# Optimization experiments

Measured on AMD Instinct MI355X. Metric: run time of the kernel, lower is better.

## Reference

```python
import jax, jax.numpy as jnp
import numpy as np
import math

NUM_HEADS = 8

def _ln(x, g, b, eps=1e-5):
    mu = x.mean(-1, keepdims=True)
    var = ((x - mu) ** 2).mean(-1, keepdims=True)
    return (x - mu) / jnp.sqrt(var + eps) * g + b

def setup_inputs() -> dict:
    key = jax.random.key(0)
    ks = jax.random.split(key, 10)
    B, Nq, Nk, dQ, dK, dV = 16, 1024, 1024, 512, 512, 512
    s = 0.05  # small init so the double-exp in masked_softmax stays finite
    Q = jax.random.normal(ks[0], (B, Nq, dQ), jnp.float32)
    K = jax.random.normal(ks[1], (B, Nk, dK), jnp.float32)
    Qm = (jax.random.uniform(ks[2], (B, Nq, 1)) < 0.9).astype(jnp.float32)
    Km = (jax.random.uniform(ks[3], (B, Nk, 1)) < 0.9).astype(jnp.float32)
    Wq = jax.random.normal(ks[4], (dQ, dV), jnp.float32) * s
    Wk = jax.random.normal(ks[5], (dK, dV), jnp.float32) * s
    Wv = jax.random.normal(ks[6], (dK, dV), jnp.float32) * s
    Wo = jax.random.normal(ks[7], (dV, dV), jnp.float32) * s
    bq = jnp.zeros((dV,), jnp.float32); bk = jnp.zeros((dV,), jnp.float32)
    bv = jnp.zeros((dV,), jnp.float32); bo = jnp.zeros((dV,), jnp.float32)
    g0 = jnp.ones((dV,), jnp.float32); b0 = jnp.zeros((dV,), jnp.float32)
    g1 = jnp.ones((dV,), jnp.float32); b1 = jnp.zeros((dV,), jnp.float32)
    return {"Q": Q, "K": K, "Qm": Qm, "Km": Km,
            "Wq": Wq, "bq": bq, "Wk": Wk, "bk": bk, "Wv": Wv, "bv": bv,
            "Wo": Wo, "bo": bo, "g0": g0, "b0": b0, "g1": g1, "b1": b1}

def reference(Q, K, Qm, Km, Wq, bq, Wk, bk, Wv, bv, Wo, bo, g0, b0, g1, b1):
    B, Nq, _ = Q.shape
    Nk = K.shape[1]
    dV = Wq.shape[1]
    h = NUM_HEADS
    dh = dV // h
    # projections + feature masking (Qm/Km broadcast over feature dim)
    Qp = (Q @ Wq + bq) * Qm          # [B,Nq,dV]
    Kp = (K @ Wk + bk) * Km          # [B,Nk,dV]
    V  = K @ Wv + bv                 # [B,Nk,dV]
    # head split: torch.cat(split(dh,2),0) == head-major [h,B,N,dh]
    Qh = Qp.reshape(B, Nq, h, dh).transpose(2, 0, 1, 3)
    Kh = Kp.reshape(B, Nk, h, dh).transpose(2, 0, 1, 3)
    Vh = V.reshape(B, Nk, h, dh).transpose(2, 0, 1, 3)
    S = jnp.einsum('hbqd,hbkd->hbqk', Qh, Kh) / math.sqrt(dV)
    # faithful masked_softmax: exp applied twice (Km branch then Qm branch)
    X = jnp.exp(S) * Km[:, :, 0][None, :, None, :]   # [h,B,Nq,Nk]
    X = jnp.exp(X) * Qm[:, :, 0][None, :, :, None]
    A = X / (X.sum(-1, keepdims=True) + 1e-8)
    O = Qh + jnp.einsum('hbqk,hbkd->hbqd', A, Vh)    # residual in head space
    O = O.transpose(1, 2, 0, 3).reshape(B, Nq, dV)   # merge heads back
    O = _ln(O, g0, b0)
    O = O + jax.nn.relu(O @ Wo + bo)
    return _ln(O, g1, b1)
```

## Files before the change

kernel.cpp:

```cpp
#include <hip/hip_runtime.h>
#include <hip/hip_bf16.h>
#include <cstdint>


typedef __bf16 bf16;
typedef __bf16 bf16x4 __attribute__((ext_vector_type(4)));
typedef __bf16 bf16x8 __attribute__((ext_vector_type(8)));
typedef float f32x4 __attribute__((ext_vector_type(4)));

#define MFMA16(a, b, c) __builtin_amdgcn_mfma_f32_16x16x32_bf16((a), (b), (c), 0, 0, 0)

#if __has_builtin(__builtin_amdgcn_exp2f)
#define EXP2F(x) __builtin_amdgcn_exp2f(x)
#else
#define EXP2F(x) exp2f(x)
#endif

static __device__ __forceinline__ void async_lds16(const bf16* g, bf16* l) {
  __builtin_amdgcn_global_load_lds(
      (__attribute__((address_space(1))) void*)(void*)g,
      (__attribute__((address_space(3))) void*)l,
      16, 0, 0);
}

__global__ __launch_bounds__(256) void transposeW(
    const float* __restrict__ Wq, const float* __restrict__ Wk,
    const float* __restrict__ Wv, const float* __restrict__ Wo,
    bf16* __restrict__ Tq, bf16* __restrict__ Tk,
    bf16* __restrict__ Tv, bf16* __restrict__ To) {
  const float* src;
  bf16* dst;
  switch (blockIdx.z) {
    case 0: src = Wq; dst = Tq; break;
    case 1: src = Wk; dst = Tk; break;
    case 2: src = Wv; dst = Tv; break;
    default: src = Wo; dst = To; break;
  }
  __shared__ bf16 t[64][72];
  const int tid = threadIdx.x;
  const int n0 = blockIdx.x * 64;
  const int k0 = blockIdx.y * 64;
  for (int c = tid; c < 512; c += 256) {
    const int row = c >> 3, col = (c & 7) * 8;
    const float* sp = src + (size_t)(k0 + row) * 512 + n0 + col;
    const f32x4 a = *(const f32x4*)sp;
    const f32x4 b = *(const f32x4*)(sp + 4);
    bf16x8 v;
#pragma unroll
    for (int j = 0; j < 4; ++j) { v[j] = (bf16)a[j]; v[j + 4] = (bf16)b[j]; }
    *(bf16x8*)(&t[row][col]) = v;
  }
  __syncthreads();
  for (int c = tid; c < 512; c += 256) {
    const int row = c >> 3, col8 = (c & 7) * 8;
    bf16x8 v;
#pragma unroll
    for (int j = 0; j < 8; ++j) v[j] = t[col8 + j][row];
    *(bf16x8*)(dst + (size_t)(n0 + row) * 512 + k0 + col8) = v;
  }
}

struct ConvArgs {
  const float* src[10];
  bf16* dst[10];
  int n[10];
};

__global__ __launch_bounds__(256) void convert_all(ConvArgs a) {
  const int seg = blockIdx.z;
  const int n = a.n[seg];
  const long i = ((long)blockIdx.x * 256 + threadIdx.x) * 8;
  if (i >= n) return;
  const float* s = a.src[seg];
  const f32x4 x0 = *(const f32x4*)(s + i);
  const f32x4 x1 = *(const f32x4*)(s + i + 4);
  bf16x8 o;
#pragma unroll
  for (int j = 0; j < 4; ++j) { o[j] = (bf16)x0[j]; o[j + 4] = (bf16)x1[j]; }
  *(bf16x8*)(a.dst[seg] + i) = o;
}

template <bool AF32>
__global__ __launch_bounds__(256, 2) void gemm512(
    const void* __restrict__ A, const bf16* __restrict__ Bt,
    const bf16* __restrict__ bias, const bf16* __restrict__ mask,
    const bf16* __restrict__ resid, bf16* __restrict__ out) {
  __shared__ bf16 sA[128 * 32];
  __shared__ bf16 sB[128 * 32];
  const int tid = threadIdx.x;
  const int lane = tid & 63;
  const int w = tid >> 6;
  const int fm = lane & 15;
  const int fq = lane >> 4;
  const long rowBase = (long)blockIdx.y * 128;
  const int colBase = blockIdx.x * 128;

  f32x4 acc[4][4] = {};

  const int c0 = tid, c1 = tid + 256;
  const int r0 = c0 >> 2, o0 = (c0 & 3) * 8;
  const int r1 = c1 >> 2, o1 = (c1 & 3) * 8;
  const bf16* A0 = (const bf16*)A + (rowBase + r0) * 512 + o0;
  const bf16* A1 = (const bf16*)A + (rowBase + r1) * 512 + o1;
  const float* F0 = (const float*)A + (rowBase + r0) * 512 + o0;
  const float* F1 = (const float*)A + (rowBase + r1) * 512 + o1;
  const bf16* B0 = Bt + (size_t)(colBase + r0) * 512 + o0;
  const bf16* B1 = Bt + (size_t)(colBase + r1) * 512 + o1;

  const int wr = (w & 1) * 64;
  const int wc = (w >> 1) * 64;

  f32x4 nx0, nx1, ny0, ny1;
  if (AF32) {
    nx0 = *(const f32x4*)(F0);
    nx1 = *(const f32x4*)(F0 + 4);
    ny0 = *(const f32x4*)(F1);
    ny1 = *(const f32x4*)(F1 + 4);
  }

  for (int kt = 0; kt < 16; ++kt) {
    const int k0 = kt * 32;
    __syncthreads();
    if (AF32) {
      bf16x8 p, q;
#pragma unroll
      for (int j = 0; j < 4; ++j) {
        p[j] = (bf16)nx0[j]; p[j + 4] = (bf16)nx1[j];
        q[j] = (bf16)ny0[j]; q[j + 4] = (bf16)ny1[j];
      }
      *(bf16x8*)(sA + c0 * 8) = p;
      *(bf16x8*)(sA + c1 * 8) = q;
      if (kt < 15) {
        nx0 = *(const f32x4*)(F0 + k0 + 32);
        nx1 = *(const f32x4*)(F0 + k0 + 36);
        ny0 = *(const f32x4*)(F1 + k0 + 32);
        ny1 = *(const f32x4*)(F1 + k0 + 36);
      }
    } else {
      async_lds16(A0 + k0, sA + c0 * 8);
      async_lds16(A1 + k0, sA + c1 * 8);
    }
    async_lds16(B0 + k0, sB + c0 * 8);
    async_lds16(B1 + k0, sB + c1 * 8);
    __syncthreads();
    bf16x8 a[4], b[4];
#pragma unroll
    for (int i = 0; i < 4; ++i)
      a[i] = *(const bf16x8*)(sA + (wr + i * 16 + fm) * 32 + fq * 8);
#pragma unroll
    for (int j = 0; j < 4; ++j)
      b[j] = *(const bf16x8*)(sB + (wc + j * 16 + fm) * 32 + fq * 8);
#pragma unroll
    for (int i = 0; i < 4; ++i)
#pragma unroll
      for (int j = 0; j < 4; ++j)
        acc[i][j] = MFMA16(a[i], b[j], acc[i][j]);
  }

#pragma unroll
  for (int i = 0; i < 4; ++i) {
#pragma unroll
    for (int r = 0; r < 4; ++r) {
      const long R = rowBase + wr + i * 16 + fq * 4 + r;
      const float mk = mask ? (float)mask[R] : 1.0f;
      const bf16* resrow = resid ? resid + R * 512 : nullptr;
      bf16* outrow = out + R * 512;
#pragma unroll
      for (int j = 0; j < 4; ++j) {
        const int C = colBase + wc + j * 16 + fm;
        float v = acc[i][j][r] + (float)bias[C];
        if (mask) v *= mk;
        if (resid) v = (float)resrow[C] + fmaxf(v, 0.0f);
        outrow[C] = (bf16)v;
      }
    }
  }
}

__global__ __launch_bounds__(256, 2) void gemmKV(
    const float* __restrict__ A, const bf16* __restrict__ Btk,
    const bf16* __restrict__ Btv, const bf16* __restrict__ bk,
    const bf16* __restrict__ bv, const bf16* __restrict__ Km,
    bf16* __restrict__ Kp, bf16* __restrict__ Vt) {
  __shared__ bf16 sA[128 * 32];
  __shared__ bf16 sBk[128 * 32];
  __shared__ bf16 sBv[128 * 32];
  const int tid = threadIdx.x;
  const int lane = tid & 63;
  const int w = tid >> 6;
  const int fm = lane & 15;
  const int fq = lane >> 4;
  const long rowBase = (long)blockIdx.y * 128;
  const int colBase = blockIdx.x * 128;

  f32x4 acck[4][4] = {};
  f32x4 accv[4][4] = {};

  const int c0 = tid, c1 = tid + 256;
  const int r0 = c0 >> 2, o0 = (c0 & 3) * 8;
  const int r1 = c1 >> 2, o1 = (c1 & 3) * 8;
  const float* F0 = A + (rowBase + r0) * 512 + o0;
  const float* F1 = A + (rowBase + r1) * 512 + o1;
  const bf16* Bk0 = Btk + (size_t)(colBase + r0) * 512 + o0;
  const bf16* Bk1 = Btk + (size_t)(colBase + r1) * 512 + o1;
  const bf16* Bv0 = Btv + (size_t)(colBase + r0) * 512 + o0;
  const bf16* Bv1 = Btv + (size_t)(colBase + r1) * 512 + o1;

  const int wr = (w & 1) * 64;
  const int wc = (w >> 1) * 64;

  f32x4 nx0 = *(const f32x4*)(F0);
  f32x4 nx1 = *(const f32x4*)(F0 + 4);
  f32x4 ny0 = *(const f32x4*)(F1);
  f32x4 ny1 = *(const f32x4*)(F1 + 4);

  for (int kt = 0; kt < 16; ++kt) {
    const int k0 = kt * 32;
    __syncthreads();
    {
      bf16x8 p, q;
#pragma unroll
      for (int j = 0; j < 4; ++j) {
        p[j] = (bf16)nx0[j]; p[j + 4] = (bf16)nx1[j];
        q[j] = (bf16)ny0[j]; q[j + 4] = (bf16)ny1[j];
      }
      *(bf16x8*)(sA + c0 * 8) = p;
      *(bf16x8*)(sA + c1 * 8) = q;
      if (kt < 15) {
        nx0 = *(const f32x4*)(F0 + k0 + 32);
        nx1 = *(const f32x4*)(F0 + k0 + 36);
        ny0 = *(const f32x4*)(F1 + k0 + 32);
        ny1 = *(const f32x4*)(F1 + k0 + 36);
      }
    }
    async_lds16(Bk0 + k0, sBk + c0 * 8);
    async_lds16(Bk1 + k0, sBk + c1 * 8);
    async_lds16(Bv0 + k0, sBv + c0 * 8);
    async_lds16(Bv1 + k0, sBv + c1 * 8);
    __syncthreads();
    bf16x8 a[4], b[4], bv2[4];
#pragma unroll
    for (int i = 0; i < 4; ++i)
      a[i] = *(const bf16x8*)(sA + (wr + i * 16 + fm) * 32 + fq * 8);
#pragma unroll
    for (int j = 0; j < 4; ++j) {
      b[j] = *(const bf16x8*)(sBk + (wc + j * 16 + fm) * 32 + fq * 8);
      bv2[j] = *(const bf16x8*)(sBv + (wc + j * 16 + fm) * 32 + fq * 8);
    }
#pragma unroll
    for (int i = 0; i < 4; ++i)
#pragma unroll
      for (int j = 0; j < 4; ++j) {
        acck[i][j] = MFMA16(a[i], b[j], acck[i][j]);
        accv[i][j] = MFMA16(a[i], bv2[j], accv[i][j]);
      }
  }

  const int bidx = (int)(rowBase >> 10);
#pragma unroll
  for (int i = 0; i < 4; ++i) {
#pragma unroll
    for (int r = 0; r < 4; ++r) {
      const long R = rowBase + wr + i * 16 + fq * 4 + r;
      const float mk = (float)Km[R];
      bf16* outrow = Kp + R * 512;
#pragma unroll
      for (int j = 0; j < 4; ++j) {
        const int C = colBase + wc + j * 16 + fm;
        outrow[C] = (bf16)((acck[i][j][r] + (float)bk[C]) * mk);
      }
    }
    const int kkb = (int)(rowBase & 1023) + wr + i * 16 + fq * 4;
#pragma unroll
    for (int j = 0; j < 4; ++j) {
      const int C = colBase + wc + j * 16 + fm;
      const float bvc = (float)bv[C];
      bf16x4 pv;
#pragma unroll
      for (int r = 0; r < 4; ++r) pv[r] = (bf16)(accv[i][j][r] + bvc);
      bf16* dst = Vt + ((size_t)(bidx * 8 + (C >> 6)) * 64 + (C & 63)) * 1024 + kkb;
      *(bf16x4*)((void*)dst) = pv;
    }
  }
}

__global__ __launch_bounds__(256) void attn_kernel(
    bf16* __restrict__ Qp, const bf16* __restrict__ Kp,
    const bf16* __restrict__ Vt, const bf16* __restrict__ Qm,
    const bf16* __restrict__ Km) {
  __shared__ bf16 sQ[64][72];
  __shared__ bf16 sK[64][72];
  __shared__ bf16 sVt[64][72];
  __shared__ bf16 sX[4][16][72];
  __shared__ float sKl[64];
  __shared__ float sL[4][16];

  const int tid = threadIdx.x;
  const int lane = tid & 63;
  const int w = tid >> 6;
  const int fm = lane & 15;
  const int fq = lane >> 4;
  const int id = blockIdx.x;
  const int bh = id & 127;
  const int q0 = (id >> 7) * 64;
  const int b = bh >> 3;
  const int hh = bh & 7;

  bf16* Qbase = Qp + ((long)b * 1024 + q0) * 512 + hh * 64;
  for (int c = tid; c < 512; c += 256) {
    const int row = c >> 3, col = (c & 7) * 8;
    *(bf16x8*)(&sQ[row][col]) = *(const bf16x8*)(Qbase + (long)row * 512 + col);
  }
  const float qm_lane = (float)Qm[(long)b * 1024 + q0 + w * 16 + fm];
  __syncthreads();

  bf16x8 qf[2];
  qf[0] = *(const bf16x8*)(&sQ[w * 16 + fm][fq * 8]);
  qf[1] = *(const bf16x8*)(&sQ[w * 16 + fm][32 + fq * 8]);

  f32x4 acc_o[4] = {};
  float l_lane = 0.f;
  const float c1 = 0.063758715f;
  const float LOG2E = 1.4426950408889634f;

  const bf16* Vthead = Vt + ((long)b * 8 + hh) * 64 * 1024;
  const bf16* Kbb = Kp + (long)b * 1024 * 512 + hh * 64;
  const bf16* Kmb = Km + (long)b * 1024;

  for (int kt = 0; kt < 16; ++kt) {
    const int kk0 = kt * 64;
    __syncthreads();
    const bf16* Kbase = Kbb + (long)kk0 * 512;
    for (int c = tid; c < 512; c += 256) {
      const int row = c >> 3, col = (c & 7) * 8;
      *(bf16x8*)(&sK[row][col]) = *(const bf16x8*)(Kbase + (long)row * 512 + col);
      *(bf16x8*)(&sVt[row][col]) =
          *(const bf16x8*)(Vthead + (long)row * 1024 + kk0 + col);
    }
    if (tid < 64) sKl[tid] = (float)Kmb[kk0 + tid] * LOG2E;
    __syncthreads();

    f32x4 s_acc[4] = {};
#pragma unroll
    for (int ks = 0; ks < 2; ++ks)
#pragma unroll
      for (int t = 0; t < 4; ++t) {
        const bf16x8 kf = *(const bf16x8*)(&sK[t * 16 + fm][ks * 32 + fq * 8]);
        s_acc[t] = MFMA16(kf, qf[ks], s_acc[t]);
      }
#pragma unroll
    for (int t = 0; t < 4; ++t) {
      const f32x4 kml4 = *(const f32x4*)(&sKl[t * 16 + fq * 4]);
      bf16x4 xp;
#pragma unroll
      for (int r = 0; r < 4; ++r) {
        const float e1 = EXP2F(s_acc[t][r] * c1);
        const float y = EXP2F(e1 * kml4[r]);
        l_lane += y;
        xp[r] = (bf16)y;
      }
      *(bf16x4*)((void*)&sX[w][fm][t * 16 + fq * 4]) = xp;
    }
#pragma unroll
    for (int ks = 0; ks < 2; ++ks) {
      const bf16x8 xf = *(const bf16x8*)(&sX[w][fm][ks * 32 + fq * 8]);
#pragma unroll
      for (int t = 0; t < 4; ++t) {
        const bf16x8 vf = *(const bf16x8*)(&sVt[t * 16 + fm][ks * 32 + fq * 8]);
        acc_o[t] = MFMA16(xf, vf, acc_o[t]);
      }
    }
  }

  l_lane += __shfl_xor(l_lane, 16);
  l_lane += __shfl_xor(l_lane, 32);
  if (fq == 0) sL[w][fm] = l_lane;

#pragma unroll
  for (int t = 0; t < 4; ++t) {
#pragma unroll
    for (int r = 0; r < 4; ++r) {
      const int qr = w * 16 + fq * 4 + r;
      const int dc = t * 16 + fm;
      const float qm_r = __shfl(qm_lane, fq * 4 + r, 64);
      const float li = 1.0f / (qm_r * sL[w][fq * 4 + r] + 1e-8f);
      const float val = (float)sQ[qr][dc] + qm_r * acc_o[t][r] * li;
      Qbase[(long)qr * 512 + dc] = (bf16)val;
    }
  }
}

__global__ __launch_bounds__(256) void lnorm(
    const bf16* __restrict__ X, const bf16* __restrict__ g,
    const bf16* __restrict__ bb, bf16* __restrict__ out) {
  const int row = blockIdx.x * 4 + (threadIdx.x >> 6);
  const int lane = threadIdx.x & 63;
  const bf16x8 v = *(const bf16x8*)(X + (size_t)row * 512 + lane * 8);
  float x[8], s = 0.f, ss = 0.f;
#pragma unroll
  for (int j = 0; j < 8; ++j) {
    x[j] = (float)v[j];
    s += x[j];
    ss += x[j] * x[j];
  }
#pragma unroll
  for (int m = 1; m < 64; m <<= 1) {
    s += __shfl_xor(s, m);
    ss += __shfl_xor(ss, m);
  }
  const float mean = s * (1.0f / 512.0f);
  const float var = ss * (1.0f / 512.0f) - mean * mean;
  const float rstd = 1.0f / sqrtf(var + 1e-5f);
  const bf16x8 gv = *(const bf16x8*)(g + lane * 8);
  const bf16x8 bv = *(const bf16x8*)(bb + lane * 8);
  bf16x8 o;
#pragma unroll
  for (int j = 0; j < 8; ++j)
    o[j] = (bf16)((x[j] - mean) * rstd * (float)gv[j] + (float)bv[j]);
  *(bf16x8*)(out + (size_t)row * 512 + lane * 8) = o;
}

__global__ __launch_bounds__(256) void lnorm_out(
    const bf16* __restrict__ X, const bf16* __restrict__ g,
    const bf16* __restrict__ bb, float* __restrict__ out) {
  const int row = blockIdx.x * 4 + (threadIdx.x >> 6);
  const int lane = threadIdx.x & 63;
  const bf16x8 v = *(const bf16x8*)(X + (size_t)row * 512 + lane * 8);
  float x[8], s = 0.f, ss = 0.f;
#pragma unroll
  for (int j = 0; j < 8; ++j) {
    x[j] = (float)v[j];
    s += x[j];
    ss += x[j] * x[j];
  }
#pragma unroll
  for (int m = 1; m < 64; m <<= 1) {
    s += __shfl_xor(s, m);
    ss += __shfl_xor(ss, m);
  }
  const float mean = s * (1.0f / 512.0f);
  const float var = ss * (1.0f / 512.0f) - mean * mean;
  const float rstd = 1.0f / sqrtf(var + 1e-5f);
  const bf16x8 gv = *(const bf16x8*)(g + lane * 8);
  const bf16x8 bv = *(const bf16x8*)(bb + lane * 8);
  f32x4 a, c;
#pragma unroll
  for (int j = 0; j < 4; ++j) {
    a[j] = (x[j] - mean) * rstd * (float)gv[j] + (float)bv[j];
    c[j] = (x[j + 4] - mean) * rstd * (float)gv[j + 4] + (float)bv[j + 4];
  }
  float* fo = out + (size_t)row * 512 + lane * 8;
  *(f32x4*)fo = a;
  *(f32x4*)(fo + 4) = c;
}

extern "C" void kernel_launch(void* const* d_in, const int* in_sizes, int n_in,
                              void* d_out, int out_size, void* d_ws, size_t ws_size,
                              hipStream_t stream) {
  (void)in_sizes; (void)n_in; (void)out_size; (void)ws_size;
  const float* Q = (const float*)d_in[0];
  const float* K = (const float*)d_in[1];

  bf16* ws = (bf16*)d_ws;
  const long W2 = 512L * 512;
  const long MN = 16384L * 512;
  bf16* Tq = ws;
  bf16* Tk = Tq + W2;
  bf16* Tv = Tk + W2;
  bf16* To = Tv + W2;
  bf16* sm = To + W2;
  bf16* cQm = sm + 8 * 512;
  bf16* cKm = cQm + 16384;
  bf16* Qp = cKm + 16384;
  bf16* Kp = Qp + MN;
  bf16* Vt = (bf16*)d_out;

  bf16* cbq = sm + 0 * 512;
  bf16* cbk = sm + 1 * 512;
  bf16* cbv = sm + 2 * 512;
  bf16* cbo = sm + 3 * 512;
  bf16* cg0 = sm + 4 * 512;
  bf16* cb0 = sm + 5 * 512;
  bf16* cg1 = sm + 6 * 512;
  bf16* cb1 = sm + 7 * 512;

  transposeW<<<dim3(8, 8, 4), 256, 0, stream>>>(
      (const float*)d_in[4], (const float*)d_in[6],
      (const float*)d_in[8], (const float*)d_in[10], Tq, Tk, Tv, To);

  ConvArgs ca;
  ca.src[0] = (const float*)d_in[2];  ca.dst[0] = cQm; ca.n[0] = 16384;
  ca.src[1] = (const float*)d_in[3];  ca.dst[1] = cKm; ca.n[1] = 16384;
  ca.src[2] = (const float*)d_in[5];  ca.dst[2] = cbq; ca.n[2] = 512;
  ca.src[3] = (const float*)d_in[7];  ca.dst[3] = cbk; ca.n[3] = 512;
  ca.src[4] = (const float*)d_in[9];  ca.dst[4] = cbv; ca.n[4] = 512;
  ca.src[5] = (const float*)d_in[11]; ca.dst[5] = cbo; ca.n[5] = 512;
  ca.src[6] = (const float*)d_in[12]; ca.dst[6] = cg0; ca.n[6] = 512;
  ca.src[7] = (const float*)d_in[13]; ca.dst[7] = cb0; ca.n[7] = 512;
  ca.src[8] = (const float*)d_in[14]; ca.dst[8] = cg1; ca.n[8] = 512;
  ca.src[9] = (const float*)d_in[15]; ca.dst[9] = cb1; ca.n[9] = 512;
  convert_all<<<dim3(8, 1, 10), 256, 0, stream>>>(ca);

  const dim3 gg(4, 128);
  gemm512<true><<<gg, 256, 0, stream>>>(Q, Tq, cbq, cQm, nullptr, Qp);
  gemmKV<<<gg, 256, 0, stream>>>(K, Tk, Tv, cbk, cbv, cKm, Kp, Vt);

  attn_kernel<<<2048, 256, 0, stream>>>(Qp, Kp, Vt, cQm, cKm);

  lnorm<<<4096, 256, 0, stream>>>(Qp, cg0, cb0, Qp);
  gemm512<false><<<gg, 256, 0, stream>>>(Qp, To, cbo, nullptr, Qp, Kp);
  lnorm_out<<<4096, 256, 0, stream>>>(Kp, cg1, cb1, (float*)d_out);
}
```

Before: 311.4 us.

## Pre-convert inputs to bf16, swizzle GEMM tiles, double attention query tile

A separate kernel now converts Q and K from fp32 to bf16 up front, so the projection GEMMs can load A through asynchronous global-to-LDS copies instead of converting inside the loop in registers. The GEMM blocks use a swizzled 1-D grid so that neighbouring blocks share A rows for better L2 reuse. The attention kernel processes 128 query rows per block (32 per wave) so each K/V tile loaded into LDS serves twice as many queries. The cost is an extra full read and write of Q and K in bf16, plus higher register and LDS use in the attention kernel.

```diff
diff --git a/kernel.cpp b/kernel.cpp
--- a/kernel.cpp
+++ b/kernel.cpp
@@ -21,6 +21,11 @@
       (__attribute__((address_space(1))) void*)(void*)g,
       (__attribute__((address_space(3))) void*)l,
       16, 0, 0);
+}
+
+static __device__ __forceinline__ void swz512(int id, long& rowBase, int& colBase) {
+  colBase = ((id >> 3) & 3) * 128;
+  rowBase = (long)((id & 7) + 8 * (id >> 5)) * 128;
 }
 
 __global__ __launch_bounds__(256) void transposeW(
@@ -60,6 +65,20 @@
   }
 }
 
+__global__ __launch_bounds__(256) void convertX(
+    const float* __restrict__ Q, const float* __restrict__ K,
+    bf16* __restrict__ Qb, bf16* __restrict__ Kb) {
+  const float* s = blockIdx.y ? K : Q;
+  bf16* d = blockIdx.y ? Kb : Qb;
+  const long i = ((long)blockIdx.x * 256 + threadIdx.x) * 8;
+  const f32x4 x0 = *(const f32x4*)(s + i);
+  const f32x4 x1 = *(const f32x4*)(s + i + 4);
+  bf16x8 o;
+#pragma unroll
+  for (int j = 0; j < 4; ++j) { o[j] = (bf16)x0[j]; o[j + 4] = (bf16)x1[j]; }
+  *(bf16x8*)(d + i) = o;
+}
+
 struct ConvArgs {
   const float* src[10];
   bf16* dst[10];
@@ -80,9 +99,8 @@
   *(bf16x8*)(a.dst[seg] + i) = o;
 }
 
-template <bool AF32>
 __global__ __launch_bounds__(256, 2) void gemm512(
-    const void* __restrict__ A, const bf16* __restrict__ Bt,
+    const bf16* __restrict__ A, const bf16* __restrict__ Bt,
     const bf16* __restrict__ bias, const bf16* __restrict__ mask,
     const bf16* __restrict__ resid, bf16* __restrict__ out) {
   __shared__ bf16 sA[128 * 32];
@@ -92,54 +110,27 @@
   const int w = tid >> 6;
   const int fm = lane & 15;
   const int fq = lane >> 4;
-  const long rowBase = (long)blockIdx.y * 128;
-  const int colBase = blockIdx.x * 128;
+  long rowBase; int colBase;
+  swz512(blockIdx.x, rowBase, colBase);
 
   f32x4 acc[4][4] = {};
 
   const int c0 = tid, c1 = tid + 256;
   const int r0 = c0 >> 2, o0 = (c0 & 3) * 8;
   const int r1 = c1 >> 2, o1 = (c1 & 3) * 8;
-  const bf16* A0 = (const bf16*)A + (rowBase + r0) * 512 + o0;
-  const bf16* A1 = (const bf16*)A + (rowBase + r1) * 512 + o1;
-  const float* F0 = (const float*)A + (rowBase + r0) * 512 + o0;
-  const float* F1 = (const float*)A + (rowBase + r1) * 512 + o1;
+  const bf16* A0 = A + (rowBase + r0) * 512 + o0;
+  const bf16* A1 = A + (rowBase + r1) * 512 + o1;
   const bf16* B0 = Bt + (size_t)(colBase + r0) * 512 + o0;
   const bf16* B1 = Bt + (size_t)(colBase + r1) * 512 + o1;
 
   const int wr = (w & 1) * 64;
   const int wc = (w >> 1) * 64;
-
-  f32x4 nx0, nx1, ny0, ny1;
-  if (AF32) {
-    nx0 = *(const f32x4*)(F0);
-    nx1 = *(const f32x4*)(F0 + 4);
-    ny0 = *(const f32x4*)(F1);
-    ny1 = *(const f32x4*)(F1 + 4);
-  }
 
   for (int kt = 0; kt < 16; ++kt) {
     const int k0 = kt * 32;
     __syncthreads();
-    if (AF32) {
-      bf16x8 p, q;
-#pragma unroll
-      for (int j = 0; j < 4; ++j) {
-        p[j] = (bf16)nx0[j]; p[j + 4] = (bf16)nx1[j];
-        q[j] = (bf16)ny0[j]; q[j + 4] = (bf16)ny1[j];
-      }
-      *(bf16x8*)(sA + c0 * 8) = p;
-      *(bf16x8*)(sA + c1 * 8) = q;
-      if (kt < 15) {
-        nx0 = *(const f32x4*)(F0 + k0 + 32);
-        nx1 = *(const f32x4*)(F0 + k0 + 36);
-        ny0 = *(const f32x4*)(F1 + k0 + 32);
-        ny1 = *(const f32x4*)(F1 + k0 + 36);
-      }
-    } else {
-      async_lds16(A0 + k0, sA + c0 * 8);
-      async_lds16(A1 + k0, sA + c1 * 8);
-    }
+    async_lds16(A0 + k0, sA + c0 * 8);
+    async_lds16(A1 + k0, sA + c1 * 8);
     async_lds16(B0 + k0, sB + c0 * 8);
     async_lds16(B1 + k0, sB + c1 * 8);
     __syncthreads();
@@ -178,7 +169,7 @@
 }
 
 __global__ __launch_bounds__(256, 2) void gemmKV(
-    const float* __restrict__ A, const bf16* __restrict__ Btk,
+    const bf16* __restrict__ A, const bf16* __restrict__ Btk,
     const bf16* __restrict__ Btv, const bf16* __restrict__ bk,
     const bf16* __restrict__ bv, const bf16* __restrict__ Km,
     bf16* __restrict__ Kp, bf16* __restrict__ Vt) {
@@ -190,8 +181,8 @@
   const int w = tid >> 6;
   const int fm = lane & 15;
   const int fq = lane >> 4;
-  const long rowBase = (long)blockIdx.y * 128;
-  const int colBase = blockIdx.x * 128;
+  long rowBase; int colBase;
+  swz512(blockIdx.x, rowBase, colBase);
 
   f32x4 acck[4][4] = {};
   f32x4 accv[4][4] = {};
@@ -199,8 +190,8 @@
   const int c0 = tid, c1 = tid + 256;
   const int r0 = c0 >> 2, o0 = (c0 & 3) * 8;
   const int r1 = c1 >> 2, o1 = (c1 & 3) * 8;
-  const float* F0 = A + (rowBase + r0) * 512 + o0;
-  const float* F1 = A + (rowBase + r1) * 512 + o1;
+  const bf16* A0 = A + (rowBase + r0) * 512 + o0;
+  const bf16* A1 = A + (rowBase + r1) * 512 + o1;
   const bf16* Bk0 = Btk + (size_t)(colBase + r0) * 512 + o0;
   const bf16* Bk1 = Btk + (size_t)(colBase + r1) * 512 + o1;
   const bf16* Bv0 = Btv + (size_t)(colBase + r0) * 512 + o0;
@@ -209,30 +200,11 @@
   const int wr = (w & 1) * 64;
   const int wc = (w >> 1) * 64;
 
-  f32x4 nx0 = *(const f32x4*)(F0);
-  f32x4 nx1 = *(const f32x4*)(F0 + 4);
-  f32x4 ny0 = *(const f32x4*)(F1);
-  f32x4 ny1 = *(const f32x4*)(F1 + 4);
-
   for (int kt = 0; kt < 16; ++kt) {
     const int k0 = kt * 32;
     __syncthreads();
-    {
-      bf16x8 p, q;
-#pragma unroll
-      for (int j = 0; j < 4; ++j) {
-        p[j] = (bf16)nx0[j]; p[j + 4] = (bf16)nx1[j];
-        q[j] = (bf16)ny0[j]; q[j + 4] = (bf16)ny1[j];
-      }
-      *(bf16x8*)(sA + c0 * 8) = p;
-      *(bf16x8*)(sA + c1 * 8) = q;
-      if (kt < 15) {
-        nx0 = *(const f32x4*)(F0 + k0 + 32);
-        nx1 = *(const f32x4*)(F0 + k0 + 36);
-        ny0 = *(const f32x4*)(F1 + k0 + 32);
-        ny1 = *(const f32x4*)(F1 + k0 + 36);
-      }
-    }
+    async_lds16(A0 + k0, sA + c0 * 8);
+    async_lds16(A1 + k0, sA + c1 * 8);
     async_lds16(Bk0 + k0, sBk + c0 * 8);
     async_lds16(Bk1 + k0, sBk + c1 * 8);
     async_lds16(Bv0 + k0, sBv + c0 * 8);
@@ -284,16 +256,16 @@
   }
 }
 
-__global__ __launch_bounds__(256) void attn_kernel(
+__global__ __launch_bounds__(256, 2) void attn_kernel(
     bf16* __restrict__ Qp, const bf16* __restrict__ Kp,
     const bf16* __restrict__ Vt, const bf16* __restrict__ Qm,
     const bf16* __restrict__ Km) {
-  __shared__ bf16 sQ[64][72];
+  __shared__ bf16 sQ[128][72];
   __shared__ bf16 sK[64][72];
   __shared__ bf16 sVt[64][72];
-  __shared__ bf16 sX[4][16][72];
+  __shared__ bf16 sX[4][32][72];
   __shared__ float sKl[64];
-  __shared__ float sL[4][16];
+  __shared__ float sL[4][32];
 
   const int tid = threadIdx.x;
   const int lane = tid & 63;
@@ -302,24 +274,29 @@
   const int fq = lane >> 4;
   const int id = blockIdx.x;
   const int bh = id & 127;
-  const int q0 = (id >> 7) * 64;
+  const int q0 = (id >> 7) * 128;
   const int b = bh >> 3;
   const int hh = bh & 7;
 
   bf16* Qbase = Qp + ((long)b * 1024 + q0) * 512 + hh * 64;
-  for (int c = tid; c < 512; c += 256) {
+  for (int c = tid; c < 1024; c += 256) {
     const int row = c >> 3, col = (c & 7) * 8;
     *(bf16x8*)(&sQ[row][col]) = *(const bf16x8*)(Qbase + (long)row * 512 + col);
   }
-  const float qm_lane = (float)Qm[(long)b * 1024 + q0 + w * 16 + fm];
+  float qm_lane[2];
+  qm_lane[0] = (float)Qm[(long)b * 1024 + q0 + w * 32 + fm];
+  qm_lane[1] = (float)Qm[(long)b * 1024 + q0 + w * 32 + 16 + fm];
   __syncthreads();
 
-  bf16x8 qf[2];
-  qf[0] = *(const bf16x8*)(&sQ[w * 16 + fm][fq * 8]);
-  qf[1] = *(const bf16x8*)(&sQ[w * 16 + fm][32 + fq * 8]);
-
-  f32x4 acc_o[4] = {};
-  float l_lane = 0.f;
+  bf16x8 qf[2][2];
+#pragma unroll
+  for (int u = 0; u < 2; ++u)
+#pragma unroll
+    for (int ks = 0; ks < 2; ++ks)
+      qf[u][ks] = *(const bf16x8*)(&sQ[w * 32 + u * 16 + fm][ks * 32 + fq * 8]);
+
+  f32x4 acc_o[2][4] = {};
+  float l_lane[2] = {0.f, 0.f};
   const float c1 = 0.063758715f;
   const float LOG2E = 1.4426950408889634f;
 
@@ -340,52 +317,63 @@
     if (tid < 64) sKl[tid] = (float)Kmb[kk0 + tid] * LOG2E;
     __syncthreads();
 
-    f32x4 s_acc[4] = {};
+    f32x4 s_acc[2][4] = {};
 #pragma unroll
     for (int ks = 0; ks < 2; ++ks)
 #pragma unroll
       for (int t = 0; t < 4; ++t) {
         const bf16x8 kf = *(const bf16x8*)(&sK[t * 16 + fm][ks * 32 + fq * 8]);
-        s_acc[t] = MFMA16(kf, qf[ks], s_acc[t]);
-      }
-#pragma unroll
-    for (int t = 0; t < 4; ++t) {
-      const f32x4 kml4 = *(const f32x4*)(&sKl[t * 16 + fq * 4]);
-      bf16x4 xp;
-#pragma unroll
-      for (int r = 0; r < 4; ++r) {
-        const float e1 = EXP2F(s_acc[t][r] * c1);
-        const float y = EXP2F(e1 * kml4[r]);
-        l_lane += y;
-        xp[r] = (bf16)y;
-      }
-      *(bf16x4*)((void*)&sX[w][fm][t * 16 + fq * 4]) = xp;
-    }
+        s_acc[0][t] = MFMA16(kf, qf[0][ks], s_acc[0][t]);
+        s_acc[1][t] = MFMA16(kf, qf[1][ks], s_acc[1][t]);
+      }
+#pragma unroll
+    for (int u = 0; u < 2; ++u)
+#pragma unroll
+      for (int t = 0; t < 4; ++t) {
+        const f32x4 kml4 = *(const f32x4*)(&sKl[t * 16 + fq * 4]);
+        bf16x4 xp;
+#pragma unroll
+        for (int r = 0; r < 4; ++r) {
+          const float e1 = EXP2F(s_acc[u][t][r] * c1);
+          const float y = EXP2F(e1 * kml4[r]);
+          l_lane[u] += y;
+          xp[r] = (bf16)y;
+        }
+        *(bf16x4*)((void*)&sX[w][u * 16 + fm][t * 16 + fq * 4]) = xp;
+      }
 #pragma unroll
     for (int ks = 0; ks < 2; ++ks) {
-      const bf16x8 xf = *(const bf16x8*)(&sX[w][fm][ks * 32 + fq * 8]);
+      const bf16x8 xf0 = *(const bf16x8*)(&sX[w][fm][ks * 32 + fq * 8]);
+      const bf16x8 xf1 = *(const bf16x8*)(&sX[w][16 + fm][ks * 32 + fq * 8]);
 #pragma unroll
       for (int t = 0; t < 4; ++t) {
         const bf16x8 vf = *(const bf16x8*)(&sVt[t * 16 + fm][ks * 32 + fq * 8]);
-        acc_o[t] = MFMA16(xf, vf, acc_o[t]);
-      }
-    }
-  }
-
-  l_lane += __shfl_xor(l_lane, 16);
-  l_lane += __shfl_xor(l_lane, 32);
-  if (fq == 0) sL[w][fm] = l_lane;
-
-#pragma unroll
-  for (int t = 0; t < 4; ++t) {
-#pragma unroll
-    for (int r = 0; r < 4; ++r) {
-      const int qr = w * 16 + fq * 4 + r;
-      const int dc = t * 16 + fm;
-      const float qm_r = __shfl(qm_lane, fq * 4 + r, 64);
-      const float li = 1.0f / (qm_r * sL[w][fq * 4 + r] + 1e-8f);
-      const float val = (float)sQ[qr][dc] + qm_r * acc_o[t][r] * li;
-      Qbase[(long)qr * 512 + dc] = (bf16)val;
+        acc_o[0][t] = MFMA16(xf0, vf, acc_o[0][t]);
+        acc_o[1][t] = MFMA16(xf1, vf, acc_o[1][t]);
+      }
+    }
+  }
+
+#pragma unroll
+  for (int u = 0; u < 2; ++u) {
+    l_lane[u] += __shfl_xor(l_lane[u], 16);
+    l_lane[u] += __shfl_xor(l_lane[u], 32);
+    if (fq == 0) sL[w][u * 16 + fm] = l_lane[u];
+  }
+
+#pragma unroll
+  for (int u = 0; u < 2; ++u) {
+#pragma unroll
+    for (int t = 0; t < 4; ++t) {
+#pragma unroll
+      for (int r = 0; r < 4; ++r) {
+        const int qr = w * 32 + u * 16 + fq * 4 + r;
+        const int dc = t * 16 + fm;
+        const float qm_r = __shfl(qm_lane[u], fq * 4 + r, 64);
+        const float li = 1.0f / (qm_r * sL[w][u * 16 + fq * 4 + r] + 1e-8f);
+        const float val = (float)sQ[qr][dc] + qm_r * acc_o[u][t][r] * li;
+        Qbase[(long)qr * 512 + dc] = (bf16)val;
+      }
     }
   }
 }
@@ -473,7 +461,9 @@
   bf16* cKm = cQm + 16384;
   bf16* Qp = cKm + 16384;
   bf16* Kp = Qp + MN;
-  bf16* Vt = (bf16*)d_out;
+  bf16* Qbf = Kp;
+  bf16* Kbf = (bf16*)d_out;
+  bf16* Vt = (bf16*)d_out + MN;
 
   bf16* cbq = sm + 0 * 512;
   bf16* cbk = sm + 1 * 512;
@@ -501,13 +491,14 @@
   ca.src[9] = (const float*)d_in[15]; ca.dst[9] = cb1; ca.n[9] = 512;
   convert_all<<<dim3(8, 1, 10), 256, 0, stream>>>(ca);
 
-  const dim3 gg(4, 128);
-  gemm512<true><<<gg, 256, 0, stream>>>(Q, Tq, cbq, cQm, nullptr, Qp);
-  gemmKV<<<gg, 256, 0, stream>>>(K, Tk, Tv, cbk, cbv, cKm, Kp, Vt);
-
-  attn_kernel<<<2048, 256, 0, stream>>>(Qp, Kp, Vt, cQm, cKm);
+  convertX<<<dim3(4096, 2), 256, 0, stream>>>(Q, K, Qbf, Kbf);
+
+  gemm512<<<512, 256, 0, stream>>>(Qbf, Tq, cbq, cQm, nullptr, Qp);
+  gemmKV<<<512, 256, 0, stream>>>(Kbf, Tk, Tv, cbk, cbv, cKm, Kp, Vt);
+
+  attn_kernel<<<1024, 256, 0, stream>>>(Qp, Kp, Vt, cQm, cKm);
 
   lnorm<<<4096, 256, 0, stream>>>(Qp, cg0, cb0, Qp);
-  gemm512<false><<<gg, 256, 0, stream>>>(Qp, To, cbo, nullptr, Qp, Kp);
+  gemm512<<<512, 256, 0, stream>>>(Qp, To, cbo, nullptr, Qp, Kp);
   lnorm_out<<<4096, 256, 0, stream>>>(Kp, cg1, cb1, (float*)d_out);
 }
```

Result: faster. 293.6 us (-5.7%).
